# Kernel tuning notes

Hardware: AMD Instinct MI355X
Metric: run time of the kernel (lower is better)

The kernel has to match this reference:

```python
import jax, jax.numpy as jnp
import numpy as np

PY_SIZES = [256, 64]
BASE = 256


def _resize_bilinear_ac(x, out):
    # NCHW bilinear resize, align_corners=True (matches F.interpolate(..., align_corners=True))
    def interp(x, axis, in_size):
        pos = jnp.arange(out, dtype=jnp.float32) * (in_size - 1) / (out - 1)
        lo = jnp.floor(pos).astype(jnp.int32)
        hi = jnp.minimum(lo + 1, in_size - 1)
        w = (pos - lo.astype(jnp.float32)).astype(x.dtype)
        shp = [1] * x.ndim
        shp[axis] = out
        w = w.reshape(shp)
        return jnp.take(x, lo, axis=axis) * (1 - w) + jnp.take(x, hi, axis=axis) * w
    x = interp(x, 2, x.shape[2])
    x = interp(x, 3, x.shape[3])
    return x


def _area_pool(x, f):
    # F.interpolate(mode='area') for integer downscale factor f == average pooling
    B, C, H, W = x.shape
    return x.reshape(B, C, H // f, f, W // f, f).mean(axis=(3, 5))


def _nearest_up_int(x, out):
    # F.interpolate(mode='nearest'): src = floor(dst * in/out)
    h = x.shape[2]
    idx = (jnp.arange(out) * h) // out
    return x[:, :, idx][:, :, :, idx]


def _buffers(B):
    grids, lin_ids, img_ids = [], [], []
    prev = 0
    for S in PY_SIZES:
        d = jnp.arange(S, dtype=jnp.float32) + 0.5
        gy, gx = jnp.meshgrid(d, d, indexing='ij')
        grids.append(jnp.broadcast_to(jnp.stack([gy, gx], -1)[None, None], (B, 1, S, S, 2)))
        lin_ids.append(jnp.arange(B * S * S, dtype=jnp.int32).reshape(B, 1, S, S) + prev)
        prev += B * S * S
        img_ids.append(jnp.broadcast_to(jnp.arange(B, dtype=jnp.float32)[:, None, None, None], (B, 1, S, S)))
    return grids, lin_ids, img_ids


def setup_inputs():
    key = jax.random.key(0)
    k1, k2 = jax.random.split(key)
    b_edges = (jax.random.uniform(k1, (64, 1, 512, 512)) < 0.08).astype(jnp.float32)
    sobel = jax.random.normal(k2, (64, 2, 512, 512), dtype=jnp.float32)
    return {"b_edges": b_edges, "sobel": sobel}


def reference(b_edges, sobel):
    B = b_edges.shape[0]
    grids, lin_ids, img_ids = _buffers(B)
    # resize post-Canny maps to base pyramid level
    e0 = jnp.clip(_resize_bilinear_ac(b_edges, BASE), 0, 1)
    s0 = _resize_bilinear_ac(sobel, BASE)
    py = [(e0, s0)]
    for S in PY_SIZES[1:]:
        f = BASE // S
        py.append((_area_pool(e0, f), _area_pool(s0, f)))
    p_lin, my_lin, centers, norms, sizes, imgid = [], [], [], [], [], []
    for i, (e, s) in enumerate(py):
        S = e.shape[2]
        idx = jnp.nonzero((e != 0).reshape(-1))[0]  # stream compaction of edge pixels
        if i + 1 < len(py):
            pl = _nearest_up_int(lin_ids[i + 1], S).reshape(-1)[idx]
        else:
            pl = lin_ids[i].reshape(-1)[idx]
        rat = BASE / S
        p_lin.append(pl)
        my_lin.append(lin_ids[i].reshape(-1)[idx])
        centers.append(grids[i].reshape(-1, 2)[idx] * rat)
        norms.append(jnp.transpose(s, (0, 2, 3, 1)).reshape(-1, 2)[idx])
        sizes.append(jnp.full(idx.shape, rat, dtype=jnp.float32))
        imgid.append(img_ids[i].reshape(-1)[idx])
    p_lin = jnp.concatenate(p_lin)
    my_lin = jnp.concatenate(my_lin)
    centers = jnp.concatenate(centers)
    norms = jnp.concatenate(norms)
    sizes = jnp.concatenate(sizes)
    imgid = jnp.concatenate(imgid)
    # parent scatter: linid -> row of that string, then gather by parent linid
    rowids = jnp.arange(my_lin.shape[0], dtype=jnp.int32)
    table = jnp.zeros(int(p_lin.max()) + 1, dtype=jnp.int32).at[my_lin].set(rowids)
    p_rowids = table[p_lin]
    norms = norms / jnp.linalg.norm(norms, axis=1, keepdims=True)
    # cross([nx,ny,0],[0,0,1]) = (ny,-nx,0)
    rt = jnp.stack([norms[:, 1], -norms[:, 0]], -1) * (sizes[:, None] / 2)
    locs_lf = centers + rt
    locs_rt = centers - rt
    return locs_lf, locs_rt, norms, sizes, centers, imgid, p_rowids, my_lin
```

## Files before the change

### kernel.cpp

```cpp
#include <hip/hip_runtime.h>
#include <math.h>

#define OFFSET1 4194304

typedef unsigned long long u64;

__device__ __forceinline__ void ac_coef(int i, int& lo, int& hi, float& w) {
    float p = (float)(i * 511) / 255.0f;
    int l = (int)p;
    lo = l;
    hi = (l + 1 < 511) ? (l + 1) : 511;
    w = p - (float)l;
}
__device__ __forceinline__ float bilin(const float* __restrict__ img,
                                       int ly, int hy, float wy,
                                       int lx, int hx, float wx) {
    float a = img[ly * 512 + lx];
    float b = img[ly * 512 + hx];
    float c = img[hy * 512 + lx];
    float d = img[hy * 512 + hx];
    float rl = a * (1.0f - wy) + c * wy;
    float rh = b * (1.0f - wy) + d * wy;
    return rl * (1.0f - wx) + rh * wx;
}

__device__ __forceinline__ u64 expand4(unsigned v) {
    u64 x = v & 0xFFFFu;
    x = (x | (x << 24)) & 0x000000FF000000FFull;
    x = (x | (x << 12)) & 0x000F000F000F000Full;
    x = (x | (x << 6))  & 0x0303030303030303ull;
    x = (x | (x << 3))  & 0x1111111111111111ull;
    return x;
}

__global__ __launch_bounds__(256) void prep_kernel(const float* __restrict__ E,
                                                   const float* __restrict__ S,
                                                   float* __restrict__ s0,
                                                   float* __restrict__ s1,
                                                   u64* __restrict__ mask0,
                                                   u64* __restrict__ mask1,
                                                   int* __restrict__ counts0,
                                                   int* __restrict__ counts1,
                                                   int use_s0) {
    int lane = threadIdx.x & 63;
    int g = blockIdx.x * 4 + (threadIdx.x >> 6);
    int b = g >> 6, R = g & 63;
    int X = lane;

    float wx[4], cwx[4];
    #pragma unroll
    for (int j = 0; j < 4; ++j) {
        int xi = 4 * X + j;
        wx[j] = (float)(xi * 511) / 255.0f - (float)(8 * X + 2 * j);
        cwx[j] = 1.0f - wx[j];
    }

    unsigned pred = 0;
    int rc = 0;
    float acc0 = 0.0f, acc1 = 0.0f;
    const float* Eb = E + b * 262144;
    const float* Sp = S + (size_t)(b * 2) * 262144;

    #pragma unroll
    for (int r = 0; r < 4; ++r) {
        int y = 4 * R + r, ly = 2 * y;
        float wy = (float)(y * 511) / 255.0f - (float)ly;
        float cwy = 1.0f - wy;

        const float* Ep = Eb + ly * 512 + 8 * X;
        float4 eA = *(const float4*)Ep;
        float4 eB = *(const float4*)(Ep + 4);
        float4 eC = *(const float4*)(Ep + 512);
        float4 eD = *(const float4*)(Ep + 516);
        const float* Sa = Sp + ly * 512 + 8 * X;
        float4 a0 = *(const float4*)Sa;
        float4 a1 = *(const float4*)(Sa + 4);
        float4 a2 = *(const float4*)(Sa + 512);
        float4 a3 = *(const float4*)(Sa + 516);
        const float* Sb = Sa + 262144;
        float4 q0 = *(const float4*)Sb;
        float4 q1 = *(const float4*)(Sb + 4);
        float4 q2 = *(const float4*)(Sb + 512);
        float4 q3 = *(const float4*)(Sb + 516);

        float e0 = (eA.x*cwy + eC.x*wy)*cwx[0] + (eA.y*cwy + eC.y*wy)*wx[0];
        float e1 = (eA.z*cwy + eC.z*wy)*cwx[1] + (eA.w*cwy + eC.w*wy)*wx[1];
        float e2 = (eB.x*cwy + eD.x*wy)*cwx[2] + (eB.y*cwy + eD.y*wy)*wx[2];
        float e3 = (eB.z*cwy + eD.z*wy)*cwx[3] + (eB.w*cwy + eD.w*wy)*wx[3];
        bool p0 = (e0 != 0.0f), p1 = (e1 != 0.0f), p2 = (e2 != 0.0f), p3 = (e3 != 0.0f);
        pred |= (p0?1u:0u) << (4*r+0);
        pred |= (p1?1u:0u) << (4*r+1);
        pred |= (p2?1u:0u) << (4*r+2);
        pred |= (p3?1u:0u) << (4*r+3);
        u64 bl0 = __ballot(p0), bl1 = __ballot(p1), bl2 = __ballot(p2), bl3 = __ballot(p3);
        rc += __popcll(bl0) + __popcll(bl1) + __popcll(bl2) + __popcll(bl3);
        if (lane < 4) {
            unsigned w0 = (unsigned)(bl0 >> (16 * lane)) & 0xFFFFu;
            unsigned w1 = (unsigned)(bl1 >> (16 * lane)) & 0xFFFFu;
            unsigned w2 = (unsigned)(bl2 >> (16 * lane)) & 0xFFFFu;
            unsigned w3 = (unsigned)(bl3 >> (16 * lane)) & 0xFFFFu;
            mask0[b * 1024 + y * 4 + lane] =
                expand4(w0) | (expand4(w1) << 1) | (expand4(w2) << 2) | (expand4(w3) << 3);
        }

        float va0 = (a0.x*cwy + a2.x*wy)*cwx[0] + (a0.y*cwy + a2.y*wy)*wx[0];
        float va1 = (a0.z*cwy + a2.z*wy)*cwx[1] + (a0.w*cwy + a2.w*wy)*wx[1];
        float va2 = (a1.x*cwy + a3.x*wy)*cwx[2] + (a1.y*cwy + a3.y*wy)*wx[2];
        float va3 = (a1.z*cwy + a3.z*wy)*cwx[3] + (a1.w*cwy + a3.w*wy)*wx[3];
        float vb0 = (q0.x*cwy + q2.x*wy)*cwx[0] + (q0.y*cwy + q2.y*wy)*wx[0];
        float vb1 = (q0.z*cwy + q2.z*wy)*cwx[1] + (q0.w*cwy + q2.w*wy)*wx[1];
        float vb2 = (q1.x*cwy + q3.x*wy)*cwx[2] + (q1.y*cwy + q3.y*wy)*wx[2];
        float vb3 = (q1.z*cwy + q3.z*wy)*cwx[3] + (q1.w*cwy + q3.w*wy)*wx[3];
        acc0 += va0 + va1 + va2 + va3;
        acc1 += vb0 + vb1 + vb2 + vb3;
        if (use_s0) {
            float4* dst = (float4*)s0 + (size_t)(b * 256 + y) * 128 + 2 * X;
            dst[0] = make_float4(va0, vb0, va1, vb1);
            dst[1] = make_float4(va2, vb2, va3, vb3);
        }
    }

    u64 m1 = __ballot(pred != 0);
    ((float2*)s1)[g * 64 + X] = make_float2(acc0 * (1.0f / 16.0f),
                                            acc1 * (1.0f / 16.0f));
    if (lane == 0) {
        counts0[g] = rc;
        counts1[g] = __popcll(m1);
        mask1[g] = m1;
    }
}

__global__ __launch_bounds__(1024) void scan_kernel(const int* __restrict__ counts0,
                                                    int* __restrict__ offs0,
                                                    const int* __restrict__ counts1,
                                                    int* __restrict__ offs1,
                                                    int* __restrict__ totals) {
    __shared__ int wsum[16];
    int tid = threadIdx.x, lane = tid & 63, wave = tid >> 6;

    int carry = 0;
    for (int base = 0; base < 4096; base += 1024) {
        int v = counts0[base + tid];
        int inc = v;
        #pragma unroll
        for (int d = 1; d < 64; d <<= 1) {
            int t = __shfl_up(inc, (unsigned)d, 64);
            if (lane >= d) inc += t;
        }
        if (lane == 63) wsum[wave] = inc;
        __syncthreads();
        int wbase = 0;
        for (int i = 0; i < wave; ++i) wbase += wsum[i];
        int tot = 0;
        #pragma unroll
        for (int i = 0; i < 16; ++i) tot += wsum[i];
        offs0[base + tid] = carry + wbase + inc - v;
        carry += tot;
        __syncthreads();
    }
    if (tid == 0) totals[0] = carry;

    int carry1 = 0;
    for (int base = 0; base < 4096; base += 1024) {
        int v = counts1[base + tid];
        int inc = v;
        #pragma unroll
        for (int d = 1; d < 64; d <<= 1) {
            int t = __shfl_up(inc, (unsigned)d, 64);
            if (lane >= d) inc += t;
        }
        if (lane == 63) wsum[wave] = inc;
        __syncthreads();
        int wbase = 0;
        for (int i = 0; i < wave; ++i) wbase += wsum[i];
        int tot = 0;
        #pragma unroll
        for (int i = 0; i < 16; ++i) tot += wsum[i];
        offs1[base + tid] = carry1 + wbase + inc - v;
        carry1 += tot;
        __syncthreads();
    }
    if (tid == 0) totals[1] = carry1;
}

__device__ __forceinline__ void write_row(float* __restrict__ out, int N, int row,
                                          float cy, float cx, float s0v, float s1v,
                                          float half, float sz, float imgid,
                                          float prow, float mylin) {
    float len = sqrtf(s0v * s0v + s1v * s1v);
    float n0 = s0v / len, n1 = s1v / len;
    float rt0 = n1 * half, rt1 = -n0 * half;
    ((float2*)out)[row]           = make_float2(cy + rt0, cx + rt1);
    ((float2*)(out + 2 * N))[row] = make_float2(cy - rt0, cx - rt1);
    ((float2*)(out + 4 * N))[row] = make_float2(n0, n1);
    out[6 * N + row] = sz;
    ((float2*)(out + 7 * N))[row] = make_float2(cy, cx);
    out[9 * N + row] = imgid;
    out[10 * N + row] = prow;
    out[11 * N + row] = mylin;
}

__global__ __launch_bounds__(1024) void scatter1_kernel(const float* __restrict__ s1,
                                                        const u64* __restrict__ mask1,
                                                        const int* __restrict__ offs1,
                                                        const int* __restrict__ totals,
                                                        int* __restrict__ rank1,
                                                        float* __restrict__ out, int N) {
    int tid = threadIdx.x, lane = tid & 63, wave = tid >> 6;
    int g = blockIdx.x * 16 + wave;
    u64 m = mask1[g];
    bool pr = (m >> lane) & 1ull;
    if (!pr) return;
    int row = totals[0] + offs1[g] + __popcll(m & ((1ull << lane) - 1ull));
    int q = g * 64 + lane;
    rank1[q] = row;
    float2 sv = ((const float2*)s1)[q];
    int b = g >> 6, Y = g & 63, X = lane;
    float cy = ((float)Y + 0.5f) * 4.0f;
    float cx = ((float)X + 0.5f) * 4.0f;
    write_row(out, N, row, cy, cx, sv.x, sv.y, 2.0f, 4.0f, (float)b,
              (float)row, (float)(OFFSET1 + q));
}

__global__ __launch_bounds__(1024) void scatter0_kernel(const float* __restrict__ S,
                                                        const float* __restrict__ s0,
                                                        const u64* __restrict__ mask0,
                                                        const int* __restrict__ offs0,
                                                        const int* __restrict__ rank1,
                                                        float* __restrict__ out, int N,
                                                        int use_s0) {
    int tid = threadIdx.x, lane = tid & 63, wave = tid >> 6;
    int blk = blockIdx.x;
    int b = blk >> 6, R = blk & 63;
    int r = tid >> 8, x = tid & 255;
    int y = 4 * R + r;
    int p = (b << 16) + (y << 8) + x;
    u64 m = mask0[p >> 6];
    __shared__ int wc[16];
    if (lane == 0) wc[wave] = __popcll(m);
    __syncthreads();
    bool pr = (m >> lane) & 1ull;
    if (!pr) return;
    int wbase = 0;
    for (int i = 0; i < wave; ++i) wbase += wc[i];
    int row = offs0[blk] + wbase + __popcll(m & ((1ull << lane) - 1ull));

    float v0, v1;
    if (use_s0) {
        float2 sv = ((const float2*)s0)[(b * 256 + y) * 256 + x];
        v0 = sv.x; v1 = sv.y;
    } else {
        int ly, hy, lx, hx; float wy, wx;
        ac_coef(y, ly, hy, wy);
        ac_coef(x, lx, hx, wx);
        v0 = bilin(S + (size_t)(b * 2 + 0) * 262144, ly, hy, wy, lx, hx, wx);
        v1 = bilin(S + (size_t)(b * 2 + 1) * 262144, ly, hy, wy, lx, hx, wx);
    }
    float cy = (float)y + 0.5f;
    float cx = (float)x + 0.5f;
    int parent = (b << 12) + ((y >> 2) << 6) + (x >> 2);
    write_row(out, N, row, cy, cx, v0, v1, 0.5f, 1.0f, (float)b,
              (float)rank1[parent], (float)p);
}

extern "C" void kernel_launch(void* const* d_in, const int* in_sizes, int n_in,
                              void* d_out, int out_size, void* d_ws, size_t ws_size,
                              hipStream_t stream) {
    const float* E = (const float*)d_in[0];
    const float* S = (const float*)d_in[1];
    float* out = (float*)d_out;
    int N = out_size / 12;

    char* ws = (char*)d_ws;
    int*  rank1   = (int*)ws;
    int*  counts0 = (int*)(ws + 1048576);
    int*  offs0   = counts0 + 4096;
    int*  counts1 = offs0 + 4096;
    int*  offs1   = counts1 + 4096;
    int*  totals  = offs1 + 4096;
    u64*  mask0   = (u64*)(ws + 1048576 + 65536 + 64);
    u64*  mask1   = mask0 + 65536;
    float* s1 = (float*)(mask1 + 4096);
    float* s0 = s1 + 524288;
    size_t base_bytes = (size_t)((char*)(s1 + 524288) - ws);
    int use_s0 = (ws_size >= base_bytes + 8388608ull * 8ull) ? 1 : 0;

    prep_kernel<<<1024, 256, 0, stream>>>(E, S, (float*)s0, s1,
                                          mask0, mask1, counts0, counts1, use_s0);
    scan_kernel<<<1, 1024, 0, stream>>>(counts0, offs0, counts1, offs1, totals);
    scatter1_kernel<<<256, 1024, 0, stream>>>(s1, mask1, offs1, totals, rank1, out, N);
    scatter0_kernel<<<4096, 1024, 0, stream>>>(S, (const float*)s0, mask0, offs0,
                                               rank1, out, N, use_s0);
}
```

Measured before the change: 83.16 us.

## Split edge prediction from sobel pass and fuse resize with output scatter

The old prep kernel read both edge and sobel inputs, wrote a full-resolution resized sobel buffer, and two scatter kernels then reread it. Now a first kernel reads only edges to build per-lane predicate bits and counts. After the scan, a second kernel reads sobel, recomputes the bilinear resize and pooling in registers, and writes level-0 and level-1 rows straight to the output. This drops the s0 intermediate round trip and one launch. Whole 4-row groups with no edges skip their sobel reads, but each lane now holds more registers and makes serial per-lane row writes.

```diff
diff --git a/kernel.cpp b/kernel.cpp
--- a/kernel.cpp
+++ b/kernel.cpp
@@ -1,128 +1,58 @@
 #include <hip/hip_runtime.h>
 #include <math.h>
 
+
+typedef unsigned long long u64;
 #define OFFSET1 4194304
 
-typedef unsigned long long u64;
-
-__device__ __forceinline__ void ac_coef(int i, int& lo, int& hi, float& w) {
-    float p = (float)(i * 511) / 255.0f;
-    int l = (int)p;
-    lo = l;
-    hi = (l + 1 < 511) ? (l + 1) : 511;
-    w = p - (float)l;
-}
-__device__ __forceinline__ float bilin(const float* __restrict__ img,
-                                       int ly, int hy, float wy,
-                                       int lx, int hx, float wx) {
-    float a = img[ly * 512 + lx];
-    float b = img[ly * 512 + hx];
-    float c = img[hy * 512 + lx];
-    float d = img[hy * 512 + hx];
-    float rl = a * (1.0f - wy) + c * wy;
-    float rh = b * (1.0f - wy) + d * wy;
-    return rl * (1.0f - wx) + rh * wx;
-}
-
-__device__ __forceinline__ u64 expand4(unsigned v) {
-    u64 x = v & 0xFFFFu;
-    x = (x | (x << 24)) & 0x000000FF000000FFull;
-    x = (x | (x << 12)) & 0x000F000F000F000Full;
-    x = (x | (x << 6))  & 0x0303030303030303ull;
-    x = (x | (x << 3))  & 0x1111111111111111ull;
-    return x;
-}
-
-__global__ __launch_bounds__(256) void prep_kernel(const float* __restrict__ E,
-                                                   const float* __restrict__ S,
-                                                   float* __restrict__ s0,
-                                                   float* __restrict__ s1,
-                                                   u64* __restrict__ mask0,
-                                                   u64* __restrict__ mask1,
-                                                   int* __restrict__ counts0,
-                                                   int* __restrict__ counts1,
-                                                   int use_s0) {
+__global__ __launch_bounds__(256) void prepE_kernel(const float* __restrict__ E,
+                                                    unsigned short* __restrict__ pred16,
+                                                    u64* __restrict__ mask1,
+                                                    int* __restrict__ counts0,
+                                                    int* __restrict__ counts1) {
     int lane = threadIdx.x & 63;
     int g = blockIdx.x * 4 + (threadIdx.x >> 6);
     int b = g >> 6, R = g & 63;
-    int X = lane;
+
+    const float* Ep = E + b * 262144 + (8 * R) * 512 + 8 * lane;
+    float4 L[8], H[8];
+    #pragma unroll
+    for (int k = 0; k < 8; ++k) {
+        L[k] = *(const float4*)(Ep + k * 512);
+        H[k] = *(const float4*)(Ep + k * 512 + 4);
+    }
 
     float wx[4], cwx[4];
     #pragma unroll
     for (int j = 0; j < 4; ++j) {
-        int xi = 4 * X + j;
-        wx[j] = (float)(xi * 511) / 255.0f - (float)(8 * X + 2 * j);
+        int xi = 4 * lane + j;
+        wx[j] = (float)(xi * 511) / 255.0f - (float)(8 * lane + 2 * j);
         cwx[j] = 1.0f - wx[j];
     }
 
     unsigned pred = 0;
     int rc = 0;
-    float acc0 = 0.0f, acc1 = 0.0f;
-    const float* Eb = E + b * 262144;
-    const float* Sp = S + (size_t)(b * 2) * 262144;
-
     #pragma unroll
     for (int r = 0; r < 4; ++r) {
-        int y = 4 * R + r, ly = 2 * y;
-        float wy = (float)(y * 511) / 255.0f - (float)ly;
+        int y = 4 * R + r;
+        float wy = (float)(y * 511) / 255.0f - (float)(2 * y);
         float cwy = 1.0f - wy;
-
-        const float* Ep = Eb + ly * 512 + 8 * X;
-        float4 eA = *(const float4*)Ep;
-        float4 eB = *(const float4*)(Ep + 4);
-        float4 eC = *(const float4*)(Ep + 512);
-        float4 eD = *(const float4*)(Ep + 516);
-        const float* Sa = Sp + ly * 512 + 8 * X;
-        float4 a0 = *(const float4*)Sa;
-        float4 a1 = *(const float4*)(Sa + 4);
-        float4 a2 = *(const float4*)(Sa + 512);
-        float4 a3 = *(const float4*)(Sa + 516);
-        const float* Sb = Sa + 262144;
-        float4 q0 = *(const float4*)Sb;
-        float4 q1 = *(const float4*)(Sb + 4);
-        float4 q2 = *(const float4*)(Sb + 512);
-        float4 q3 = *(const float4*)(Sb + 516);
-
-        float e0 = (eA.x*cwy + eC.x*wy)*cwx[0] + (eA.y*cwy + eC.y*wy)*wx[0];
-        float e1 = (eA.z*cwy + eC.z*wy)*cwx[1] + (eA.w*cwy + eC.w*wy)*wx[1];
-        float e2 = (eB.x*cwy + eD.x*wy)*cwx[2] + (eB.y*cwy + eD.y*wy)*wx[2];
-        float e3 = (eB.z*cwy + eD.z*wy)*cwx[3] + (eB.w*cwy + eD.w*wy)*wx[3];
+        float4 lo = L[2 * r], loh = H[2 * r];
+        float4 hi = L[2 * r + 1], hih = H[2 * r + 1];
+        float e0 = (lo.x*cwy + hi.x*wy)*cwx[0] + (lo.y*cwy + hi.y*wy)*wx[0];
+        float e1 = (lo.z*cwy + hi.z*wy)*cwx[1] + (lo.w*cwy + hi.w*wy)*wx[1];
+        float e2 = (loh.x*cwy + hih.x*wy)*cwx[2] + (loh.y*cwy + hih.y*wy)*wx[2];
+        float e3 = (loh.z*cwy + hih.z*wy)*cwx[3] + (loh.w*cwy + hih.w*wy)*wx[3];
         bool p0 = (e0 != 0.0f), p1 = (e1 != 0.0f), p2 = (e2 != 0.0f), p3 = (e3 != 0.0f);
         pred |= (p0?1u:0u) << (4*r+0);
         pred |= (p1?1u:0u) << (4*r+1);
         pred |= (p2?1u:0u) << (4*r+2);
         pred |= (p3?1u:0u) << (4*r+3);
-        u64 bl0 = __ballot(p0), bl1 = __ballot(p1), bl2 = __ballot(p2), bl3 = __ballot(p3);
-        rc += __popcll(bl0) + __popcll(bl1) + __popcll(bl2) + __popcll(bl3);
-        if (lane < 4) {
-            unsigned w0 = (unsigned)(bl0 >> (16 * lane)) & 0xFFFFu;
-            unsigned w1 = (unsigned)(bl1 >> (16 * lane)) & 0xFFFFu;
-            unsigned w2 = (unsigned)(bl2 >> (16 * lane)) & 0xFFFFu;
-            unsigned w3 = (unsigned)(bl3 >> (16 * lane)) & 0xFFFFu;
-            mask0[b * 1024 + y * 4 + lane] =
-                expand4(w0) | (expand4(w1) << 1) | (expand4(w2) << 2) | (expand4(w3) << 3);
-        }
-
-        float va0 = (a0.x*cwy + a2.x*wy)*cwx[0] + (a0.y*cwy + a2.y*wy)*wx[0];
-        float va1 = (a0.z*cwy + a2.z*wy)*cwx[1] + (a0.w*cwy + a2.w*wy)*wx[1];
-        float va2 = (a1.x*cwy + a3.x*wy)*cwx[2] + (a1.y*cwy + a3.y*wy)*wx[2];
-        float va3 = (a1.z*cwy + a3.z*wy)*cwx[3] + (a1.w*cwy + a3.w*wy)*wx[3];
-        float vb0 = (q0.x*cwy + q2.x*wy)*cwx[0] + (q0.y*cwy + q2.y*wy)*wx[0];
-        float vb1 = (q0.z*cwy + q2.z*wy)*cwx[1] + (q0.w*cwy + q2.w*wy)*wx[1];
-        float vb2 = (q1.x*cwy + q3.x*wy)*cwx[2] + (q1.y*cwy + q3.y*wy)*wx[2];
-        float vb3 = (q1.z*cwy + q3.z*wy)*cwx[3] + (q1.w*cwy + q3.w*wy)*wx[3];
-        acc0 += va0 + va1 + va2 + va3;
-        acc1 += vb0 + vb1 + vb2 + vb3;
-        if (use_s0) {
-            float4* dst = (float4*)s0 + (size_t)(b * 256 + y) * 128 + 2 * X;
-            dst[0] = make_float4(va0, vb0, va1, vb1);
-            dst[1] = make_float4(va2, vb2, va3, vb3);
-        }
-    }
-
+        u64 b0 = __ballot(p0), b1 = __ballot(p1), b2 = __ballot(p2), b3 = __ballot(p3);
+        rc += __popcll(b0) + __popcll(b1) + __popcll(b2) + __popcll(b3);
+    }
     u64 m1 = __ballot(pred != 0);
-    ((float2*)s1)[g * 64 + X] = make_float2(acc0 * (1.0f / 16.0f),
-                                            acc1 * (1.0f / 16.0f));
+    pred16[g * 64 + lane] = (unsigned short)pred;
     if (lane == 0) {
         counts0[g] = rc;
         counts1[g] = __popcll(m1);
@@ -200,67 +130,100 @@
     out[11 * N + row] = mylin;
 }
 
-__global__ __launch_bounds__(1024) void scatter1_kernel(const float* __restrict__ s1,
-                                                        const u64* __restrict__ mask1,
-                                                        const int* __restrict__ offs1,
-                                                        const int* __restrict__ totals,
-                                                        int* __restrict__ rank1,
-                                                        float* __restrict__ out, int N) {
-    int tid = threadIdx.x, lane = tid & 63, wave = tid >> 6;
-    int g = blockIdx.x * 16 + wave;
-    u64 m = mask1[g];
-    bool pr = (m >> lane) & 1ull;
-    if (!pr) return;
-    int row = totals[0] + offs1[g] + __popcll(m & ((1ull << lane) - 1ull));
-    int q = g * 64 + lane;
-    rank1[q] = row;
-    float2 sv = ((const float2*)s1)[q];
-    int b = g >> 6, Y = g & 63, X = lane;
-    float cy = ((float)Y + 0.5f) * 4.0f;
-    float cx = ((float)X + 0.5f) * 4.0f;
-    write_row(out, N, row, cy, cx, sv.x, sv.y, 2.0f, 4.0f, (float)b,
-              (float)row, (float)(OFFSET1 + q));
-}
-
-__global__ __launch_bounds__(1024) void scatter0_kernel(const float* __restrict__ S,
-                                                        const float* __restrict__ s0,
-                                                        const u64* __restrict__ mask0,
-                                                        const int* __restrict__ offs0,
-                                                        const int* __restrict__ rank1,
-                                                        float* __restrict__ out, int N,
-                                                        int use_s0) {
-    int tid = threadIdx.x, lane = tid & 63, wave = tid >> 6;
-    int blk = blockIdx.x;
-    int b = blk >> 6, R = blk & 63;
-    int r = tid >> 8, x = tid & 255;
-    int y = 4 * R + r;
-    int p = (b << 16) + (y << 8) + x;
-    u64 m = mask0[p >> 6];
-    __shared__ int wc[16];
-    if (lane == 0) wc[wave] = __popcll(m);
-    __syncthreads();
-    bool pr = (m >> lane) & 1ull;
-    if (!pr) return;
-    int wbase = 0;
-    for (int i = 0; i < wave; ++i) wbase += wc[i];
-    int row = offs0[blk] + wbase + __popcll(m & ((1ull << lane) - 1ull));
-
-    float v0, v1;
-    if (use_s0) {
-        float2 sv = ((const float2*)s0)[(b * 256 + y) * 256 + x];
-        v0 = sv.x; v1 = sv.y;
-    } else {
-        int ly, hy, lx, hx; float wy, wx;
-        ac_coef(y, ly, hy, wy);
-        ac_coef(x, lx, hx, wx);
-        v0 = bilin(S + (size_t)(b * 2 + 0) * 262144, ly, hy, wy, lx, hx, wx);
-        v1 = bilin(S + (size_t)(b * 2 + 1) * 262144, ly, hy, wy, lx, hx, wx);
-    }
-    float cy = (float)y + 0.5f;
-    float cx = (float)x + 0.5f;
-    int parent = (b << 12) + ((y >> 2) << 6) + (x >> 2);
-    write_row(out, N, row, cy, cx, v0, v1, 0.5f, 1.0f, (float)b,
-              (float)rank1[parent], (float)p);
+__global__ __launch_bounds__(256) void prepS_kernel(const float* __restrict__ S,
+                                                    const unsigned short* __restrict__ pred16,
+                                                    const u64* __restrict__ mask1,
+                                                    const int* __restrict__ offs0,
+                                                    const int* __restrict__ offs1,
+                                                    const int* __restrict__ totals,
+                                                    float* __restrict__ out, int N) {
+    int lane = threadIdx.x & 63;
+    int g = blockIdx.x * 4 + (threadIdx.x >> 6);
+    int bimg = g >> 6, R = g & 63;
+
+    u64 m1 = mask1[g];
+    if (m1 == 0ull) return;
+    unsigned pred = pred16[g * 64 + lane];
+    int base0 = offs0[g];
+    int prow = totals[0] + offs1[g] + __popcll(m1 & ((1ull << lane) - 1ull));
+
+    float wx[4], cwx[4];
+    #pragma unroll
+    for (int j = 0; j < 4; ++j) {
+        int xi = 4 * lane + j;
+        wx[j] = (float)(xi * 511) / 255.0f - (float)(8 * lane + 2 * j);
+        cwx[j] = 1.0f - wx[j];
+    }
+
+    const float* Sa = S + (size_t)(2 * bimg) * 262144 + (8 * R) * 512 + 8 * lane;
+    const float* Sq = Sa + 262144;
+
+    float acc0 = 0.0f, acc1 = 0.0f;
+    int rc = 0;
+    #pragma unroll
+    for (int h = 0; h < 2; ++h) {
+        float4 A[4], Ax[4], Q[4], Qx[4];
+        #pragma unroll
+        for (int k = 0; k < 4; ++k) {
+            const float* pa = Sa + (4 * h + k) * 512;
+            A[k]  = *(const float4*)pa;
+            Ax[k] = *(const float4*)(pa + 4);
+            const float* pq = Sq + (4 * h + k) * 512;
+            Q[k]  = *(const float4*)pq;
+            Qx[k] = *(const float4*)(pq + 4);
+        }
+        #pragma unroll
+        for (int rr = 0; rr < 2; ++rr) {
+            int r = 2 * h + rr;
+            int y = 4 * R + r;
+            float wy = (float)(y * 511) / 255.0f - (float)(2 * y);
+            float cwy = 1.0f - wy;
+            float4 lo = A[2*rr], loh = Ax[2*rr], hi = A[2*rr+1], hih = Ax[2*rr+1];
+            float4 ql = Q[2*rr], qlh = Qx[2*rr], qh = Q[2*rr+1], qhh = Qx[2*rr+1];
+            float va[4], vb[4];
+            va[0] = (lo.x*cwy + hi.x*wy)*cwx[0] + (lo.y*cwy + hi.y*wy)*wx[0];
+            va[1] = (lo.z*cwy + hi.z*wy)*cwx[1] + (lo.w*cwy + hi.w*wy)*wx[1];
+            va[2] = (loh.x*cwy + hih.x*wy)*cwx[2] + (loh.y*cwy + hih.y*wy)*wx[2];
+            va[3] = (loh.z*cwy + hih.z*wy)*cwx[3] + (loh.w*cwy + hih.w*wy)*wx[3];
+            vb[0] = (ql.x*cwy + qh.x*wy)*cwx[0] + (ql.y*cwy + qh.y*wy)*wx[0];
+            vb[1] = (ql.z*cwy + qh.z*wy)*cwx[1] + (ql.w*cwy + qh.w*wy)*wx[1];
+            vb[2] = (qlh.x*cwy + qhh.x*wy)*cwx[2] + (qlh.y*cwy + qhh.y*wy)*wx[2];
+            vb[3] = (qlh.z*cwy + qhh.z*wy)*cwx[3] + (qlh.w*cwy + qhh.w*wy)*wx[3];
+            acc0 += va[0] + va[1] + va[2] + va[3];
+            acc1 += vb[0] + vb[1] + vb[2] + vb[3];
+
+            unsigned pr = (pred >> (4 * r)) & 0xF;
+            u64 b0 = __ballot(pr & 1);
+            u64 b1 = __ballot(pr & 2);
+            u64 b2 = __ballot(pr & 4);
+            u64 b3 = __ballot(pr & 8);
+            u64 ltm = (1ull << lane) - 1ull;
+            int pre = __popcll(b0 & ltm) + __popcll(b1 & ltm) +
+                      __popcll(b2 & ltm) + __popcll(b3 & ltm);
+            int rbase = base0 + rc + pre;
+            int own = 0;
+            #pragma unroll
+            for (int j = 0; j < 4; ++j) {
+                if (pr & (1u << j)) {
+                    int row = rbase + own;
+                    own++;
+                    int x = 4 * lane + j;
+                    float cy = (float)y + 0.5f, cx = (float)x + 0.5f;
+                    write_row(out, N, row, cy, cx, va[j], vb[j], 0.5f, 1.0f,
+                              (float)bimg, (float)prow,
+                              (float)((bimg << 16) + (y << 8) + x));
+                }
+            }
+            rc += __popcll(b0) + __popcll(b1) + __popcll(b2) + __popcll(b3);
+        }
+    }
+
+    if (pred != 0) {
+        float v0 = acc0 * (1.0f / 16.0f), v1 = acc1 * (1.0f / 16.0f);
+        float cy = ((float)R + 0.5f) * 4.0f, cx = ((float)lane + 0.5f) * 4.0f;
+        write_row(out, N, prow, cy, cx, v0, v1, 2.0f, 4.0f, (float)bimg,
+                  (float)prow, (float)(OFFSET1 + g * 64 + lane));
+    }
 }
 
 extern "C" void kernel_launch(void* const* d_in, const int* in_sizes, int n_in,
@@ -272,23 +235,16 @@
     int N = out_size / 12;
 
     char* ws = (char*)d_ws;
-    int*  rank1   = (int*)ws;
-    int*  counts0 = (int*)(ws + 1048576);
-    int*  offs0   = counts0 + 4096;
-    int*  counts1 = offs0 + 4096;
-    int*  offs1   = counts1 + 4096;
-    int*  totals  = offs1 + 4096;
-    u64*  mask0   = (u64*)(ws + 1048576 + 65536 + 64);
-    u64*  mask1   = mask0 + 65536;
-    float* s1 = (float*)(mask1 + 4096);
-    float* s0 = s1 + 524288;
-    size_t base_bytes = (size_t)((char*)(s1 + 524288) - ws);
-    int use_s0 = (ws_size >= base_bytes + 8388608ull * 8ull) ? 1 : 0;
-
-    prep_kernel<<<1024, 256, 0, stream>>>(E, S, (float*)s0, s1,
-                                          mask0, mask1, counts0, counts1, use_s0);
+    int* counts0 = (int*)(ws + 0);
+    int* offs0   = (int*)(ws + 16384);
+    int* counts1 = (int*)(ws + 32768);
+    int* offs1   = (int*)(ws + 49152);
+    int* totals  = (int*)(ws + 65536);
+    u64* mask1   = (u64*)(ws + 65600);
+    unsigned short* pred16 = (unsigned short*)(ws + 98368);
+
+    prepE_kernel<<<1024, 256, 0, stream>>>(E, pred16, mask1, counts0, counts1);
     scan_kernel<<<1, 1024, 0, stream>>>(counts0, offs0, counts1, offs1, totals);
-    scatter1_kernel<<<256, 1024, 0, stream>>>(s1, mask1, offs1, totals, rank1, out, N);
-    scatter0_kernel<<<4096, 1024, 0, stream>>>(S, (const float*)s0, mask0, offs0,
-                                               rank1, out, N, use_s0);
-}
+    prepS_kernel<<<1024, 256, 0, stream>>>(S, pred16, mask1, offs0, offs1,
+                                           totals, out, N);
+}
```

Result: faster. 75.86 us (-8.8%).
